# Optimization experiments

Measured on AMD Instinct MI355X. Metric: run time of the kernel, lower is better.

## Reference

```python
import jax, jax.numpy as jnp
import numpy as np

B, S, D = 2, 2048, 2048
H, HKV, DH = 16, 4, 128   # query heads, kv heads, head dim
N_REP = H // HKV
ROPE_BASE = 10000.0


def rotate_half(x):
    x1, x2 = x[..., : DH // 2], x[..., DH // 2 :]
    return jnp.concatenate((-x2, x1), axis=-1)


def rope_tables(seq_len, dtype=jnp.float32):
    inv_freq = 1.0 / (ROPE_BASE ** (jnp.arange(0, DH, 2, dtype=jnp.float32) / DH))
    t = jnp.arange(seq_len, dtype=jnp.float32)
    freqs = jnp.outer(t, inv_freq)                 # [S, DH/2]
    emb = jnp.concatenate((freqs, freqs), axis=-1)  # [S, DH]
    return jnp.cos(emb).astype(dtype), jnp.sin(emb).astype(dtype)


def setup_inputs() -> dict:
    key = jax.random.key(0)
    k1, k2, k3, k4, k5 = jax.random.split(key, 5)
    scale = 1.0 / np.sqrt(D)
    return {
        "hidden_states": jax.random.normal(k1, (B, S, D), dtype=jnp.float32),
        "position_ids": jnp.tile(jnp.arange(S, dtype=jnp.int32)[None, :], (B, 1)),
        "wq": jax.random.normal(k2, (D, H * DH), dtype=jnp.float32) * scale,
        "wk": jax.random.normal(k3, (D, HKV * DH), dtype=jnp.float32) * scale,
        "wv": jax.random.normal(k4, (D, HKV * DH), dtype=jnp.float32) * scale,
        "wo": jax.random.normal(k5, (H * DH, D), dtype=jnp.float32) * scale,
    }


def reference(hidden_states, position_ids, wq, wk, wv, wo):
    x = hidden_states
    b, s, _ = x.shape

    # QKV projections -> [B, H(kv), S, DH]
    q = (x @ wq).reshape(b, s, H, DH).transpose(0, 2, 1, 3)
    k = (x @ wk).reshape(b, s, HKV, DH).transpose(0, 2, 1, 3)
    v = (x @ wv).reshape(b, s, HKV, DH).transpose(0, 2, 1, 3)

    # Rotary position embedding
    cos_t, sin_t = rope_tables(s, x.dtype)
    cos = cos_t[position_ids][:, None, :, :]  # [B,1,S,DH]
    sin = sin_t[position_ids][:, None, :, :]
    q = q * cos + rotate_half(q) * sin
    k = k * cos + rotate_half(k) * sin

    # GQA: repeat KV heads to match query heads
    k = jnp.repeat(k, N_REP, axis=1)  # [B,H,S,DH]
    v = jnp.repeat(v, N_REP, axis=1)

    # Causal SDPA
    scores = jnp.einsum("bhqd,bhkd->bhqk", q, k) / jnp.sqrt(
        jnp.asarray(DH, x.dtype)
    )
    causal = jnp.tril(jnp.ones((s, s), dtype=bool))
    scores = jnp.where(causal[None, None], scores, jnp.asarray(-1e9, x.dtype))
    attn = jax.nn.softmax(scores, axis=-1)
    out = jnp.einsum("bhqk,bhkd->bhqd", attn, v)  # [B,H,S,DH]

    out = out.transpose(0, 2, 1, 3).reshape(b, s, H * DH)
    return out @ wo
```

## Files before the change

### kernel.cpp

```cpp
#include <hip/hip_runtime.h>
#include <cmath>

typedef unsigned short u16;
typedef float floatx4 __attribute__((ext_vector_type(4)));
typedef short short8 __attribute__((ext_vector_type(8)));
typedef short short4v __attribute__((ext_vector_type(4)));
typedef __bf16 bf16x8 __attribute__((ext_vector_type(8)));

#define GLOBAL_AS __attribute__((address_space(1)))
#define LDS_AS __attribute__((address_space(3)))

#define S_LEN 2048
#define D_MODEL 2048
#define NH 16
#define NKV 4
#define DHEAD 128
#define SM_SCALE 0.08838834764831843f
#define K2 (SM_SCALE * 1.4426950408889634f)

__device__ __forceinline__ u16 f2bf(float f) {
    unsigned int u = __builtin_bit_cast(unsigned int, f);
    u += 0x7fffu + ((u >> 16) & 1u);
    return (u16)(u >> 16);
}
__device__ __forceinline__ u16 f2bfr(float f) {
    unsigned int u = __builtin_bit_cast(unsigned int, f);
    return (u16)((u + 0x8000u) >> 16);
}
__device__ __forceinline__ float bf2f(u16 x) {
    unsigned int u = ((unsigned int)x) << 16;
    return __builtin_bit_cast(float, u);
}
__device__ __forceinline__ floatx4 zf4() {
    floatx4 z; z[0] = 0.f; z[1] = 0.f; z[2] = 0.f; z[3] = 0.f; return z;
}
__device__ __forceinline__ floatx4 mfma16(short8 a, short8 b, floatx4 c) {
    return __builtin_amdgcn_mfma_f32_16x16x32_bf16(
        __builtin_bit_cast(bf16x8, a), __builtin_bit_cast(bf16x8, b), c, 0, 0, 0);
}
__device__ __forceinline__ floatx4 mfma16k16(short4v a, short4v b, floatx4 c) {
    return __builtin_amdgcn_mfma_f32_16x16x16bf16_1k(a, b, c, 0, 0, 0);
}
__device__ __forceinline__ void async16(const u16* g, u16* l) {
    __builtin_amdgcn_global_load_lds((GLOBAL_AS void*)g, (LDS_AS void*)l, 16, 0, 0);
}

__global__ void cast_tables_kernel(const float4* __restrict__ in, ushort4* __restrict__ out,
                                   float* __restrict__ cs_tab, float* __restrict__ sn_tab) {
    int bid = blockIdx.x;
    if (bid < 8192) {
        int i = bid * 256 + threadIdx.x;
        float4 v = in[i];
        ushort4 o;
        o.x = f2bf(v.x); o.y = f2bf(v.y); o.z = f2bf(v.z); o.w = f2bf(v.w);
        out[i] = o;
    } else {
        int idx = (bid - 8192) * 256 + threadIdx.x;
        int p = idx >> 6, jj = idx & 63;
        double e = (double)(2 * jj) / 128.0;
        double invf = pow(10000.0, -e);
        float arg = (float)p * (float)invf;
        cs_tab[idx] = (float)cos((double)arg);
        sn_tab[idx] = (float)sin((double)arg);
    }
}

__global__ void transpose_all_kernel(const float* __restrict__ wq, const float* __restrict__ wk,
                                     const float* __restrict__ wv, const float* __restrict__ wo,
                                     u16* __restrict__ Wqkv, u16* __restrict__ Wo) {
    __shared__ float tile[32][33];
    int x = blockIdx.x;
    const float* in; u16* out; int C, bx;
    if (x < 64)      { in = wq; out = Wqkv;                     C = 2048; bx = x * 32; }
    else if (x < 80) { in = wk; out = Wqkv + (size_t)2048*2048; C = 512;  bx = (x - 64) * 32; }
    else if (x < 96) { in = wv; out = Wqkv + (size_t)2560*2048; C = 512;  bx = (x - 80) * 32; }
    else             { in = wo; out = Wo;                       C = 2048; bx = (x - 96) * 32; }
    const int R = 2048;
    int tx = threadIdx.x & 31, ty = threadIdx.x >> 5;
    int by = blockIdx.y * 32;
#pragma unroll
    for (int i = 0; i < 32; i += 8)
        tile[ty + i][tx] = in[(size_t)(by + ty + i) * C + bx + tx];
    __syncthreads();
#pragma unroll
    for (int i = 0; i < 32; i += 8)
        out[(size_t)(bx + ty + i) * R + by + tx] = f2bf(tile[tx][ty + i]);
}

__global__ void rope_k_kernel(u16* __restrict__ Kb, const int* __restrict__ pos,
                              const float4* __restrict__ cs_tab,
                              const float4* __restrict__ sn_tab) {
    int idx = blockIdx.x * 256 + threadIdx.x;
    int j4 = idx & 15;
    int s = (idx >> 4) & 2047;
    int r = idx >> 15;
    int hh = r & 3, b = r >> 2;
    int p = pos[b * S_LEN + s];
    float4 cs = cs_tab[p * 16 + j4];
    float4 sn = sn_tab[p * 16 + j4];
    u16* base = Kb + (((size_t)(b * NKV + hh)) * S_LEN + s) * DHEAD + j4 * 4;
    ushort4 a = *(const ushort4*)(base);
    ushort4 c = *(const ushort4*)(base + 64);
    ushort4 oa, oc;
    float x1, x2;
    x1 = bf2f(a.x); x2 = bf2f(c.x); oa.x = f2bf(x1 * cs.x - x2 * sn.x); oc.x = f2bf(x2 * cs.x + x1 * sn.x);
    x1 = bf2f(a.y); x2 = bf2f(c.y); oa.y = f2bf(x1 * cs.y - x2 * sn.y); oc.y = f2bf(x2 * cs.y + x1 * sn.y);
    x1 = bf2f(a.z); x2 = bf2f(c.z); oa.z = f2bf(x1 * cs.z - x2 * sn.z); oc.z = f2bf(x2 * cs.z + x1 * sn.z);
    x1 = bf2f(a.w); x2 = bf2f(c.w); oa.w = f2bf(x1 * cs.w - x2 * sn.w); oc.w = f2bf(x2 * cs.w + x1 * sn.w);
    *(ushort4*)(base) = oa;
    *(ushort4*)(base + 64) = oc;
}

__device__ __forceinline__ void gemm_mainloop(const u16* __restrict__ A,
                                              const u16* __restrict__ Bt,
                                              int K, u16* ldsA, u16* ldsB,
                                              floatx4 acc[4][4]) {
    const int t = threadIdx.x;
    const int lane = t & 63, wave = t >> 6;
    const int wr = wave >> 1, wc = wave & 1;
    const int lr = lane & 15, q = lane >> 4;
    const int m0 = blockIdx.y * 128, n0 = blockIdx.x * 128;
    const int swz = lr & 7;

#pragma unroll
    for (int r = 0; r < 4; ++r)
#pragma unroll
        for (int c = 0; c < 4; ++c) acc[r][c] = zf4();

    for (int k0 = 0; k0 < K; k0 += 64) {
#pragma unroll
        for (int i = 0; i < 4; ++i) {
            int ci = i * 256 + t;
            int row = ci >> 3;
            int kc = ((ci & 7) ^ (row & 7)) << 3;
            async16(A + (size_t)(m0 + row) * K + k0 + kc, ldsA + (i * 256 + wave * 64) * 8);
            async16(Bt + (size_t)(n0 + row) * K + k0 + kc, ldsB + (i * 256 + wave * 64) * 8);
        }
        __syncthreads();
#pragma unroll
        for (int ks = 0; ks < 2; ++ks) {
            short8 af[4], bfr[4];
#pragma unroll
            for (int r = 0; r < 4; ++r)
                af[r] = *(const short8*)(ldsA + (wr * 64 + r * 16 + lr) * 64 +
                                         (((ks * 4 + q) ^ swz) << 3));
#pragma unroll
            for (int c = 0; c < 4; ++c)
                bfr[c] = *(const short8*)(ldsB + (wc * 64 + c * 16 + lr) * 64 +
                                          (((ks * 4 + q) ^ swz) << 3));
#pragma unroll
            for (int r = 0; r < 4; ++r)
#pragma unroll
                for (int c = 0; c < 4; ++c)
                    acc[r][c] = mfma16(af[r], bfr[c], acc[r][c]);
        }
        __syncthreads();
    }
}

__global__ void qkv_gemm_kernel(const u16* __restrict__ A, const u16* __restrict__ Bt,
                                u16* __restrict__ Qb, u16* __restrict__ Kb,
                                u16* __restrict__ Vt) {
    __shared__ u16 ldsA[128 * 64];
    __shared__ u16 ldsB[128 * 64];
    floatx4 acc[4][4];
    gemm_mainloop(A, Bt, D_MODEL, ldsA, ldsB, acc);

    const int t = threadIdx.x, lane = t & 63, wave = t >> 6;
    const int wr = wave >> 1, wc = wave & 1, lr = lane & 15, q = lane >> 4;
    const int m0 = blockIdx.y * 128 + wr * 64, n0 = blockIdx.x * 128 + wc * 64;
#pragma unroll
    for (int r = 0; r < 4; ++r)
#pragma unroll
        for (int c = 0; c < 4; ++c) {
            int gc = n0 + c * 16 + lr;
#pragma unroll
            for (int rr = 0; rr < 4; ++rr) {
                int grow = m0 + r * 16 + q * 4 + rr;
                int bb = grow >> 11, s = grow & 2047;
                u16 bv = f2bf(acc[r][c][rr]);
                int d = gc & 127;
                if (gc < 2048) {
                    int hh = gc >> 7;
                    Qb[(((size_t)(bb * NH + hh)) * S_LEN + s) * DHEAD + d] = bv;
                } else if (gc < 2560) {
                    int hh = (gc - 2048) >> 7;
                    Kb[(((size_t)(bb * NKV + hh)) * S_LEN + s) * DHEAD + d] = bv;
                } else {
                    int hh = (gc - 2560) >> 7;
                    int s2 = s ^ ((d & 8) >> 1);
                    Vt[(((size_t)(bb * NKV + hh)) * DHEAD + d) * S_LEN + s2] = bv;
                }
            }
        }
}

__global__ void out_gemm_kernel(const u16* __restrict__ A, const u16* __restrict__ Bt,
                                float* __restrict__ out) {
    __shared__ u16 ldsA[128 * 64];
    __shared__ u16 ldsB[128 * 64];
    floatx4 acc[4][4];
    gemm_mainloop(A, Bt, D_MODEL, ldsA, ldsB, acc);

    const int t = threadIdx.x, lane = t & 63, wave = t >> 6;
    const int wr = wave >> 1, wc = wave & 1, lr = lane & 15, q = lane >> 4;
    const int m0 = blockIdx.y * 128 + wr * 64, n0 = blockIdx.x * 128 + wc * 64;
#pragma unroll
    for (int r = 0; r < 4; ++r)
#pragma unroll
        for (int c = 0; c < 4; ++c) {
            int gc = n0 + c * 16 + lr;
#pragma unroll
            for (int rr = 0; rr < 4; ++rr) {
                int grow = m0 + r * 16 + q * 4 + rr;
                out[(size_t)grow * D_MODEL + gc] = acc[r][c][rr];
            }
        }
}

__global__ __launch_bounds__(256, 2) void fa_kernel(const u16* __restrict__ Qb,
                                                    const u16* __restrict__ Kb,
                                                    const u16* __restrict__ Vt,
                                                    u16* __restrict__ Ob,
                                                    const int* __restrict__ pos,
                                                    const float4* __restrict__ cs_tab,
                                                    const float4* __restrict__ sn_tab) {
    __shared__ u16 ldsK[2][64 * 128];
    __shared__ u16 ldsV[2][128 * 64];

    const int t = threadIdx.x, lane = t & 63, wave = t >> 6;
    const int lr = lane & 15, q = lane >> 4;
    const int swz = lr & 7;

    const int bid = blockIdx.x;
    const int bh = bid >> 4, p = bid & 15;
    const int qt0 = p, qt1 = 31 - p;
    const int b = bh >> 4, h = bh & 15;
    const int kvh = h >> 2;

    const u16* Kp = Kb + (size_t)(b * NKV + kvh) * S_LEN * DHEAD;
    const u16* Vp = Vt + (size_t)(b * NKV + kvh) * DHEAD * S_LEN;

    short8 qf0[4], qf1[4];
    auto load_rope_q = [&](int qt, short8 (&qf)[4]) {
        const u16* Qp = Qb + ((size_t)((b * NH + h) * S_LEN) + qt * 64 + wave * 16) * DHEAD;
#pragma unroll
        for (int kk = 0; kk < 4; ++kk)
            qf[kk] = *(const short8*)(Qp + (size_t)lr * DHEAD + kk * 32 + q * 8);
        const int srow = qt * 64 + wave * 16 + lr;
        const int pp = pos[b * S_LEN + srow];
#pragma unroll
        for (int kk = 0; kk < 2; ++kk)
#pragma unroll
            for (int h4 = 0; h4 < 2; ++h4) {
                float4 cs = cs_tab[pp * 16 + kk * 8 + q * 2 + h4];
                float4 sn = sn_tab[pp * 16 + kk * 8 + q * 2 + h4];
#pragma unroll
                for (int e = 0; e < 4; ++e) {
                    float cc = (&cs.x)[e], ss = (&sn.x)[e];
                    int ei = h4 * 4 + e;
                    float x1 = bf2f((u16)qf[kk][ei]);
                    float x2 = bf2f((u16)qf[kk + 2][ei]);
                    qf[kk][ei]     = (short)f2bf(x1 * cc - x2 * ss);
                    qf[kk + 2][ei] = (short)f2bf(x2 * cc + x1 * ss);
                }
            }
    };
    load_rope_q(qt0, qf0);
    load_rope_q(qt1, qf1);

    auto stage = [&](int kt, int bs) {
#pragma unroll
        for (int i = 0; i < 4; ++i) {
            int ci = i * 256 + t;
            int krow = ci >> 4, kc = ((ci & 15) ^ ((ci >> 4) & 7)) << 3;
            async16(Kp + (size_t)(kt * 64 + krow) * DHEAD + kc,
                    &ldsK[bs][(i * 256 + wave * 64) * 8]);
            int dh = ci >> 3, vc = ((ci & 7) ^ ((ci >> 3) & 7)) << 3;
            async16(Vp + (size_t)dh * S_LEN + kt * 64 + vc,
                    &ldsV[bs][(i * 256 + wave * 64) * 8]);
        }
    };

    floatx4 accO[8];
    float m_i, l_i;

    auto do_tile = [&](int kt, int qt_c, const short8 (&qfc)[4], int bs) {
        floatx4 sc[4];
        __builtin_amdgcn_s_setprio(1);
#pragma unroll
        for (int c = 0; c < 4; ++c) {
            sc[c] = zf4();
#pragma unroll
            for (int kk = 0; kk < 4; ++kk) {
                short8 kfr = *(const short8*)(&ldsK[bs][(c * 16 + lr) * DHEAD +
                                              (((kk * 4 + q) ^ swz) << 3)]);
                sc[c] = mfma16(kfr, qfc[kk], sc[c]);
            }
        }
        __builtin_amdgcn_s_setprio(0);

        if (kt == qt_c) {
            const int qrow = wave * 16 + lr;
#pragma unroll
            for (int c = 0; c < 4; ++c)
#pragma unroll
                for (int rr = 0; rr < 4; ++rr)
                    if (c * 16 + q * 4 + rr > qrow) sc[c][rr] = -3e38f;
        }

        float mx = -3e38f;
#pragma unroll
        for (int c = 0; c < 4; ++c)
#pragma unroll
            for (int rr = 0; rr < 4; ++rr) mx = fmaxf(mx, sc[c][rr]);
        mx = fmaxf(mx, __shfl_xor(mx, 16));
        mx = fmaxf(mx, __shfl_xor(mx, 32));
        float mnew = fmaxf(m_i, mx);
        float mk = mnew * K2;
        bool anyup = __any(mnew > m_i);
        float rs = 0.f;
#pragma unroll
        for (int c = 0; c < 4; ++c)
#pragma unroll
            for (int rr = 0; rr < 4; ++rr) {
                float pe = __builtin_amdgcn_exp2f(fmaf(sc[c][rr], K2, -mk));
                sc[c][rr] = pe;
                rs += pe;
            }
        rs += __shfl_xor(rs, 16);
        rs += __shfl_xor(rs, 32);
        if (anyup) {
            float alpha = __builtin_amdgcn_exp2f(fmaf(m_i, K2, -mk));
            l_i = l_i * alpha + rs;
#pragma unroll
            for (int d = 0; d < 8; ++d) accO[d] *= alpha;
        } else {
            l_i += rs;
        }
        m_i = mnew;

        short4v pb[4];
#pragma unroll
        for (int c = 0; c < 4; ++c) {
            pb[c][0] = (short)f2bfr(sc[c][0]);
            pb[c][1] = (short)f2bfr(sc[c][1]);
            pb[c][2] = (short)f2bfr(sc[c][2]);
            pb[c][3] = (short)f2bfr(sc[c][3]);
        }

        __builtin_amdgcn_s_setprio(1);
#pragma unroll
        for (int ks = 0; ks < 4; ++ks)
#pragma unroll
            for (int d = 0; d < 8; ++d) {
                short4v vf = *(const short4v*)(&ldsV[bs][(d * 16 + lr) * 64 +
                                               (((ks * 2 + (q >> 1)) ^ swz) << 3) +
                                               (((q ^ (lr >> 3)) & 1) << 2)]);
                accO[d] = mfma16k16(vf, pb[ks], accO[d]);
            }
        __builtin_amdgcn_s_setprio(0);
    };

    auto epilogue = [&](int qt_c) {
        const int tok = qt_c * 64 + wave * 16 + lr;
        const float inv = 1.0f / l_i;
        u16* orow = Ob + ((size_t)(b * S_LEN + tok)) * (NH * DHEAD) + h * DHEAD + q * 4;
#pragma unroll
        for (int d = 0; d < 8; ++d) {
            ushort4 o;
            o.x = f2bf(accO[d][0] * inv);
            o.y = f2bf(accO[d][1] * inv);
            o.z = f2bf(accO[d][2] * inv);
            o.w = f2bf(accO[d][3] * inv);
            *(ushort4*)(orow + d * 16) = o;
        }
    };

#pragma unroll
    for (int d = 0; d < 8; ++d) accO[d] = zf4();
    m_i = -3e38f; l_i = 0.f;

    int cur = 0;
    stage(0, 0);
    __syncthreads();

    for (int kt = 0; kt <= qt0; ++kt) {
        int nxt = cur ^ 1;
        int nk = (kt < qt0) ? kt + 1 : 0;
        stage(nk, nxt);
        do_tile(kt, qt0, qf0, cur);
        __syncthreads();
        cur = nxt;
    }
    epilogue(qt0);
#pragma unroll
    for (int d = 0; d < 8; ++d) accO[d] = zf4();
    m_i = -3e38f; l_i = 0.f;

    for (int kt = 0; kt <= qt1; ++kt) {
        int nxt = cur ^ 1;
        if (kt < qt1) stage(kt + 1, nxt);
        do_tile(kt, qt1, qf1, cur);
        __syncthreads();
        cur = nxt;
    }
    epilogue(qt1);
}

extern "C" void kernel_launch(void* const* d_in, const int* in_sizes, int n_in,
                              void* d_out, int out_size, void* d_ws, size_t ws_size,
                              hipStream_t stream) {
    const float* X  = (const float*)d_in[0];
    const int* pos  = (const int*)d_in[1];
    const float* wq = (const float*)d_in[2];
    const float* wk = (const float*)d_in[3];
    const float* wv = (const float*)d_in[4];
    const float* wo = (const float*)d_in[5];
    float* out = (float*)d_out;

    char* w = (char*)d_ws;
    u16* Xbf    = (u16*)(w);
    u16* Wqkv   = (u16*)(w + 16777216);
    u16* Wo     = (u16*)(w + 29360128);
    u16* Qb     = (u16*)(w + 37748736);
    u16* Kb     = (u16*)(w + 54525952);
    u16* Vt     = (u16*)(w + 58720256);
    u16* Ob     = (u16*)(w + 62914560);
    float* cst  = (float*)(w + 79691776);
    float* snt  = (float*)(w + 80216064);

    cast_tables_kernel<<<8704, 256, 0, stream>>>((const float4*)X, (ushort4*)Xbf, cst, snt);
    transpose_all_kernel<<<dim3(160, 64), 256, 0, stream>>>(wq, wk, wv, wo, Wqkv, Wo);
    qkv_gemm_kernel<<<dim3(24, 32), 256, 0, stream>>>(Xbf, Wqkv, Qb, Kb, Vt);
    rope_k_kernel<<<1024, 256, 0, stream>>>(Kb, pos, (const float4*)cst, (const float4*)snt);
    fa_kernel<<<512, 256, 0, stream>>>(Qb, Kb, Vt, Ob, pos, (const float4*)cst, (const float4*)snt);
    out_gemm_kernel<<<dim3(16, 32), 256, 0, stream>>>(Ob, Wo, out);
}
```

Baseline: 304.1 us.

## Process both query tiles in one shared KV loop to reuse staged K/V

Merges the two sequential per-query-tile KV loops into a single loop over KV tiles. Each staged K/V tile is now shared by both query tiles while the lower tile is still active, which roughly halves the K/V global loads and LDS staging for the overlapping range. The sync is also changed from __syncthreads to explicit vmcnt waits plus raw barriers, so the next tile's prefetch can stay in flight. In exchange it doubles the accumulator and score registers, which may lower occupancy, and the hand-written waitcnt counts must exactly match the outstanding async loads to stay correct.

```diff
diff --git a/kernel.cpp b/kernel.cpp
--- a/kernel.cpp
+++ b/kernel.cpp
@@ -282,33 +282,22 @@
         }
     };
 
-    floatx4 accO[8];
-    float m_i, l_i;
-
-    auto do_tile = [&](int kt, int qt_c, const short8 (&qfc)[4], int bs) {
-        floatx4 sc[4];
-        __builtin_amdgcn_s_setprio(1);
-#pragma unroll
-        for (int c = 0; c < 4; ++c) {
-            sc[c] = zf4();
-#pragma unroll
-            for (int kk = 0; kk < 4; ++kk) {
-                short8 kfr = *(const short8*)(&ldsK[bs][(c * 16 + lr) * DHEAD +
-                                              (((kk * 4 + q) ^ swz) << 3)]);
-                sc[c] = mfma16(kfr, qfc[kk], sc[c]);
-            }
-        }
-        __builtin_amdgcn_s_setprio(0);
-
-        if (kt == qt_c) {
-            const int qrow = wave * 16 + lr;
-#pragma unroll
-            for (int c = 0; c < 4; ++c)
-#pragma unroll
-                for (int rr = 0; rr < 4; ++rr)
-                    if (c * 16 + q * 4 + rr > qrow) sc[c][rr] = -3e38f;
-        }
-
+    floatx4 accO0[8], accO1[8];
+#pragma unroll
+    for (int d = 0; d < 8; ++d) { accO0[d] = zf4(); accO1[d] = zf4(); }
+    float m0v = -3e38f, l0v = 0.f, m1v = -3e38f, l1v = 0.f;
+
+    auto do_mask = [&](floatx4 (&sc)[4]) {
+        const int qrow = wave * 16 + lr;
+#pragma unroll
+        for (int c = 0; c < 4; ++c)
+#pragma unroll
+            for (int rr = 0; rr < 4; ++rr)
+                if (c * 16 + q * 4 + rr > qrow) sc[c][rr] = -3e38f;
+    };
+
+    auto softmax_pack = [&](floatx4 (&sc)[4], float& m_i, float& l_i,
+                            floatx4 (&accO)[8], short4v (&pb)[4]) {
         float mx = -3e38f;
 #pragma unroll
         for (int c = 0; c < 4; ++c)
@@ -339,8 +328,6 @@
             l_i += rs;
         }
         m_i = mnew;
-
-        short4v pb[4];
 #pragma unroll
         for (int c = 0; c < 4; ++c) {
             pb[c][0] = (short)f2bfr(sc[c][0]);
@@ -348,21 +335,84 @@
             pb[c][2] = (short)f2bfr(sc[c][2]);
             pb[c][3] = (short)f2bfr(sc[c][3]);
         }
+    };
+
+    asm volatile("s_waitcnt vmcnt(0)" ::: "memory");
+    stage(0, 0);
+    int cur = 0;
+
+    for (int kt = 0; kt <= qt1; ++kt) {
+        stage(kt < qt1 ? kt + 1 : 0, cur ^ 1);
+        asm volatile("s_waitcnt vmcnt(8)" ::: "memory");
+        __builtin_amdgcn_s_barrier();
+
+        const bool act0 = (kt <= qt0);
+        floatx4 sc0[4], sc1[4];
 
         __builtin_amdgcn_s_setprio(1);
-#pragma unroll
-        for (int ks = 0; ks < 4; ++ks)
-#pragma unroll
-            for (int d = 0; d < 8; ++d) {
-                short4v vf = *(const short4v*)(&ldsV[bs][(d * 16 + lr) * 64 +
-                                               (((ks * 2 + (q >> 1)) ^ swz) << 3) +
-                                               (((q ^ (lr >> 3)) & 1) << 2)]);
-                accO[d] = mfma16k16(vf, pb[ks], accO[d]);
-            }
+        if (act0) {
+#pragma unroll
+            for (int c = 0; c < 4; ++c) {
+                sc0[c] = zf4(); sc1[c] = zf4();
+#pragma unroll
+                for (int kk = 0; kk < 4; ++kk) {
+                    short8 kfr = *(const short8*)(&ldsK[cur][(c * 16 + lr) * DHEAD +
+                                                  (((kk * 4 + q) ^ swz) << 3)]);
+                    sc1[c] = mfma16(kfr, qf1[kk], sc1[c]);
+                    sc0[c] = mfma16(kfr, qf0[kk], sc0[c]);
+                }
+            }
+        } else {
+#pragma unroll
+            for (int c = 0; c < 4; ++c) {
+                sc1[c] = zf4();
+#pragma unroll
+                for (int kk = 0; kk < 4; ++kk) {
+                    short8 kfr = *(const short8*)(&ldsK[cur][(c * 16 + lr) * DHEAD +
+                                                  (((kk * 4 + q) ^ swz) << 3)]);
+                    sc1[c] = mfma16(kfr, qf1[kk], sc1[c]);
+                }
+            }
+        }
         __builtin_amdgcn_s_setprio(0);
-    };
-
-    auto epilogue = [&](int qt_c) {
+
+        if (kt == qt0) do_mask(sc0);
+        if (kt == qt1) do_mask(sc1);
+
+        short4v pb0[4], pb1[4];
+        softmax_pack(sc1, m1v, l1v, accO1, pb1);
+        if (act0) softmax_pack(sc0, m0v, l0v, accO0, pb0);
+
+        __builtin_amdgcn_s_setprio(1);
+        if (act0) {
+#pragma unroll
+            for (int ks = 0; ks < 4; ++ks)
+#pragma unroll
+                for (int d = 0; d < 8; ++d) {
+                    short4v vf = *(const short4v*)(&ldsV[cur][(d * 16 + lr) * 64 +
+                                                   (((ks * 2 + (q >> 1)) ^ swz) << 3) +
+                                                   (((q ^ (lr >> 3)) & 1) << 2)]);
+                    accO1[d] = mfma16k16(vf, pb1[ks], accO1[d]);
+                    accO0[d] = mfma16k16(vf, pb0[ks], accO0[d]);
+                }
+        } else {
+#pragma unroll
+            for (int ks = 0; ks < 4; ++ks)
+#pragma unroll
+                for (int d = 0; d < 8; ++d) {
+                    short4v vf = *(const short4v*)(&ldsV[cur][(d * 16 + lr) * 64 +
+                                                   (((ks * 2 + (q >> 1)) ^ swz) << 3) +
+                                                   (((q ^ (lr >> 3)) & 1) << 2)]);
+                    accO1[d] = mfma16k16(vf, pb1[ks], accO1[d]);
+                }
+        }
+        __builtin_amdgcn_s_setprio(0);
+
+        __builtin_amdgcn_s_barrier();
+        cur ^= 1;
+    }
+
+    auto epilogue = [&](int qt_c, floatx4 (&accO)[8], float l_i) {
         const int tok = qt_c * 64 + wave * 16 + lr;
         const float inv = 1.0f / l_i;
         u16* orow = Ob + ((size_t)(b * S_LEN + tok)) * (NH * DHEAD) + h * DHEAD + q * 4;
@@ -376,36 +426,9 @@
             *(ushort4*)(orow + d * 16) = o;
         }
     };
-
-#pragma unroll
-    for (int d = 0; d < 8; ++d) accO[d] = zf4();
-    m_i = -3e38f; l_i = 0.f;
-
-    int cur = 0;
-    stage(0, 0);
-    __syncthreads();
-
-    for (int kt = 0; kt <= qt0; ++kt) {
-        int nxt = cur ^ 1;
-        int nk = (kt < qt0) ? kt + 1 : 0;
-        stage(nk, nxt);
-        do_tile(kt, qt0, qf0, cur);
-        __syncthreads();
-        cur = nxt;
-    }
-    epilogue(qt0);
-#pragma unroll
-    for (int d = 0; d < 8; ++d) accO[d] = zf4();
-    m_i = -3e38f; l_i = 0.f;
-
-    for (int kt = 0; kt <= qt1; ++kt) {
-        int nxt = cur ^ 1;
-        if (kt < qt1) stage(kt + 1, nxt);
-        do_tile(kt, qt1, qf1, cur);
-        __syncthreads();
-        cur = nxt;
-    }
-    epilogue(qt1);
+    epilogue(qt0, accO0, l0v);
+    epilogue(qt1, accO1, l1v);
+    asm volatile("s_waitcnt vmcnt(0)" ::: "memory");
 }
 
 extern "C" void kernel_launch(void* const* d_in, const int* in_sizes, int n_in,
```

New measurement: 323.7 us. 6.4% more time.

## Use 128-row query tiles with 8 waves sharing K/V staging in flash attention

Applied to the files above, without the earlier changes.

The attention kernel moves from 4-wave blocks that each handled two 64-row query tiles (paired for causal balance) to 8-wave blocks that each handle one 128-row query tile. Each staged K/V tile is now shared by twice as many query rows, which halves the global-to-LDS traffic per query. Load balance now comes from reversing the tile order for half the heads rather than from pairing tiles inside a block. The causal mask is generalised to the last two key tiles. Block work is now uneven, and the larger blocks with a launch bound of 4 may restrict registers and occupancy.

```diff
diff --git a/kernel.cpp b/kernel.cpp
--- a/kernel.cpp
+++ b/kernel.cpp
@@ -218,7 +218,7 @@
         }
 }
 
-__global__ __launch_bounds__(256, 2) void fa_kernel(const u16* __restrict__ Qb,
+__global__ __launch_bounds__(512, 4) void fa_kernel(const u16* __restrict__ Qb,
                                                     const u16* __restrict__ Kb,
                                                     const u16* __restrict__ Vt,
                                                     u16* __restrict__ Ob,
@@ -233,21 +233,22 @@
     const int swz = lr & 7;
 
     const int bid = blockIdx.x;
-    const int bh = bid >> 4, p = bid & 15;
-    const int qt0 = p, qt1 = 31 - p;
+    const int bh = bid >> 4, jslot = bid & 15;
+    const int qt2 = (bh & 16) ? (15 - jslot) : jslot;
     const int b = bh >> 4, h = bh & 15;
     const int kvh = h >> 2;
 
     const u16* Kp = Kb + (size_t)(b * NKV + kvh) * S_LEN * DHEAD;
     const u16* Vp = Vt + (size_t)(b * NKV + kvh) * DHEAD * S_LEN;
-
-    short8 qf0[4], qf1[4];
-    auto load_rope_q = [&](int qt, short8 (&qf)[4]) {
-        const u16* Qp = Qb + ((size_t)((b * NH + h) * S_LEN) + qt * 64 + wave * 16) * DHEAD;
-#pragma unroll
-        for (int kk = 0; kk < 4; ++kk)
-            qf[kk] = *(const short8*)(Qp + (size_t)lr * DHEAD + kk * 32 + q * 8);
-        const int srow = qt * 64 + wave * 16 + lr;
+    const u16* Qp = Qb + ((size_t)((b * NH + h) * S_LEN) + qt2 * 128 + wave * 16) * DHEAD;
+
+    short8 qf[4];
+#pragma unroll
+    for (int kk = 0; kk < 4; ++kk)
+        qf[kk] = *(const short8*)(Qp + (size_t)lr * DHEAD + kk * 32 + q * 8);
+
+    {
+        const int srow = qt2 * 128 + wave * 16 + lr;
         const int pp = pos[b * S_LEN + srow];
 #pragma unroll
         for (int kk = 0; kk < 2; ++kk)
@@ -265,27 +266,34 @@
                     qf[kk + 2][ei] = (short)f2bf(x2 * cc + x1 * ss);
                 }
             }
+    }
+
+    auto stage = [&](int kt, int bs) {
+#pragma unroll
+        for (int i = 0; i < 2; ++i) {
+            int ci = i * 512 + t;
+            int krow = ci >> 4, kc = ((ci & 15) ^ (krow & 7)) << 3;
+            async16(Kp + (size_t)(kt * 64 + krow) * DHEAD + kc,
+                    &ldsK[bs][(i * 512 + wave * 64) * 8]);
+            int dh = ci >> 3, vc = ((ci & 7) ^ (dh & 7)) << 3;
+            async16(Vp + (size_t)dh * S_LEN + kt * 64 + vc,
+                    &ldsV[bs][(i * 512 + wave * 64) * 8]);
+        }
     };
-    load_rope_q(qt0, qf0);
-    load_rope_q(qt1, qf1);
-
-    auto stage = [&](int kt, int bs) {
-#pragma unroll
-        for (int i = 0; i < 4; ++i) {
-            int ci = i * 256 + t;
-            int krow = ci >> 4, kc = ((ci & 15) ^ ((ci >> 4) & 7)) << 3;
-            async16(Kp + (size_t)(kt * 64 + krow) * DHEAD + kc,
-                    &ldsK[bs][(i * 256 + wave * 64) * 8]);
-            int dh = ci >> 3, vc = ((ci & 7) ^ ((ci >> 3) & 7)) << 3;
-            async16(Vp + (size_t)dh * S_LEN + kt * 64 + vc,
-                    &ldsV[bs][(i * 256 + wave * 64) * 8]);
-        }
-    };
 
     floatx4 accO[8];
-    float m_i, l_i;
-
-    auto do_tile = [&](int kt, int qt_c, const short8 (&qfc)[4], int bs) {
+#pragma unroll
+    for (int d = 0; d < 8; ++d) accO[d] = zf4();
+    float m_i = -3e38f, l_i = 0.f;
+
+    const int nkt = 2 * qt2 + 2;
+    int cur = 0;
+    stage(0, 0);
+    __syncthreads();
+
+    for (int kt = 0; kt < nkt; ++kt) {
+        if (kt + 1 < nkt) stage(kt + 1, cur ^ 1);
+
         floatx4 sc[4];
         __builtin_amdgcn_s_setprio(1);
 #pragma unroll
@@ -293,20 +301,21 @@
             sc[c] = zf4();
 #pragma unroll
             for (int kk = 0; kk < 4; ++kk) {
-                short8 kfr = *(const short8*)(&ldsK[bs][(c * 16 + lr) * DHEAD +
+                short8 kfr = *(const short8*)(&ldsK[cur][(c * 16 + lr) * DHEAD +
                                               (((kk * 4 + q) ^ swz) << 3)]);
-                sc[c] = mfma16(kfr, qfc[kk], sc[c]);
+                sc[c] = mfma16(kfr, qf[kk], sc[c]);
             }
         }
         __builtin_amdgcn_s_setprio(0);
 
-        if (kt == qt_c) {
-            const int qrow = wave * 16 + lr;
+        if (kt >= 2 * qt2) {
+            const int koff = (kt - 2 * qt2) << 6;
+            const int gq = wave * 16 + lr;
 #pragma unroll
             for (int c = 0; c < 4; ++c)
 #pragma unroll
                 for (int rr = 0; rr < 4; ++rr)
-                    if (c * 16 + q * 4 + rr > qrow) sc[c][rr] = -3e38f;
+                    if (koff + c * 16 + q * 4 + rr > gq) sc[c][rr] = -3e38f;
         }
 
         float mx = -3e38f;
@@ -354,58 +363,29 @@
         for (int ks = 0; ks < 4; ++ks)
 #pragma unroll
             for (int d = 0; d < 8; ++d) {
-                short4v vf = *(const short4v*)(&ldsV[bs][(d * 16 + lr) * 64 +
+                short4v vf = *(const short4v*)(&ldsV[cur][(d * 16 + lr) * 64 +
                                                (((ks * 2 + (q >> 1)) ^ swz) << 3) +
                                                (((q ^ (lr >> 3)) & 1) << 2)]);
                 accO[d] = mfma16k16(vf, pb[ks], accO[d]);
             }
         __builtin_amdgcn_s_setprio(0);
-    };
-
-    auto epilogue = [&](int qt_c) {
-        const int tok = qt_c * 64 + wave * 16 + lr;
-        const float inv = 1.0f / l_i;
-        u16* orow = Ob + ((size_t)(b * S_LEN + tok)) * (NH * DHEAD) + h * DHEAD + q * 4;
-#pragma unroll
-        for (int d = 0; d < 8; ++d) {
-            ushort4 o;
-            o.x = f2bf(accO[d][0] * inv);
-            o.y = f2bf(accO[d][1] * inv);
-            o.z = f2bf(accO[d][2] * inv);
-            o.w = f2bf(accO[d][3] * inv);
-            *(ushort4*)(orow + d * 16) = o;
-        }
-    };
-
-#pragma unroll
-    for (int d = 0; d < 8; ++d) accO[d] = zf4();
-    m_i = -3e38f; l_i = 0.f;
-
-    int cur = 0;
-    stage(0, 0);
-    __syncthreads();
-
-    for (int kt = 0; kt <= qt0; ++kt) {
-        int nxt = cur ^ 1;
-        int nk = (kt < qt0) ? kt + 1 : 0;
-        stage(nk, nxt);
-        do_tile(kt, qt0, qf0, cur);
+
         __syncthreads();
-        cur = nxt;
+        cur ^= 1;
     }
-    epilogue(qt0);
-#pragma unroll
-    for (int d = 0; d < 8; ++d) accO[d] = zf4();
-    m_i = -3e38f; l_i = 0.f;
-
-    for (int kt = 0; kt <= qt1; ++kt) {
-        int nxt = cur ^ 1;
-        if (kt < qt1) stage(kt + 1, nxt);
-        do_tile(kt, qt1, qf1, cur);
-        __syncthreads();
-        cur = nxt;
+
+    const int tok = qt2 * 128 + wave * 16 + lr;
+    const float inv = 1.0f / l_i;
+    u16* orow = Ob + ((size_t)(b * S_LEN + tok)) * (NH * DHEAD) + h * DHEAD + q * 4;
+#pragma unroll
+    for (int d = 0; d < 8; ++d) {
+        ushort4 o;
+        o.x = f2bf(accO[d][0] * inv);
+        o.y = f2bf(accO[d][1] * inv);
+        o.z = f2bf(accO[d][2] * inv);
+        o.w = f2bf(accO[d][3] * inv);
+        *(ushort4*)(orow + d * 16) = o;
     }
-    epilogue(qt1);
 }
 
 extern "C" void kernel_launch(void* const* d_in, const int* in_sizes, int n_in,
@@ -434,6 +414,6 @@
     transpose_all_kernel<<<dim3(160, 64), 256, 0, stream>>>(wq, wk, wv, wo, Wqkv, Wo);
     qkv_gemm_kernel<<<dim3(24, 32), 256, 0, stream>>>(Xbf, Wqkv, Qb, Kb, Vt);
     rope_k_kernel<<<1024, 256, 0, stream>>>(Kb, pos, (const float4*)cst, (const float4*)snt);
-    fa_kernel<<<512, 256, 0, stream>>>(Qb, Kb, Vt, Ob, pos, (const float4*)cst, (const float4*)snt);
+    fa_kernel<<<512, 512, 0, stream>>>(Qb, Kb, Vt, Ob, pos, (const float4*)cst, (const float4*)snt);
     out_gemm_kernel<<<dim3(16, 32), 256, 0, stream>>>(Ob, Wo, out);
 }
```

New measurement: 297.9 us. 1.02x faster.

## Double-buffer GEMM mainloop with larger 8-wave tiles and MFMA priority

Applied to the files above, without the earlier changes.

Replaces the single-buffered 128x128 GEMM mainloop with a templated 8-wave version that prefetches the next K tile into a second LDS buffer while computing the current one, synchronised with explicit vmcnt waits and raw barriers. Tiles grow to 256x256 for the QKV projection and 128x256 for the output projection. MFMA blocks are wrapped in s_setprio. The aim is to hide global-load latency and raise operand reuse per block. In exchange there are fewer blocks, which can underfill the CUs (192 and 256 blocks), plus higher register pressure and hand-tuned vmcnt counts that must match the issued loads exactly.

```diff
diff --git a/kernel.cpp b/kernel.cpp
--- a/kernel.cpp
+++ b/kernel.cpp
@@ -111,66 +111,111 @@
     *(ushort4*)(base + 64) = oc;
 }
 
-__device__ __forceinline__ void gemm_mainloop(const u16* __restrict__ A,
-                                              const u16* __restrict__ Bt,
-                                              int K, u16* ldsA, u16* ldsB,
-                                              floatx4 acc[4][4]) {
+template <int M_REP>
+__device__ __forceinline__ void gemm_mainloop8(const u16* __restrict__ A,
+                                               const u16* __restrict__ Bt,
+                                               int K,
+                                               u16* ldsA0, u16* ldsB0,
+                                               u16* ldsA1, u16* ldsB1,
+                                               floatx4 acc[M_REP][4]) {
     const int t = threadIdx.x;
     const int lane = t & 63, wave = t >> 6;
-    const int wr = wave >> 1, wc = wave & 1;
+    const int wr = wave >> 2, wc = wave & 3;
     const int lr = lane & 15, q = lane >> 4;
-    const int m0 = blockIdx.y * 128, n0 = blockIdx.x * 128;
     const int swz = lr & 7;
-
-#pragma unroll
-    for (int r = 0; r < 4; ++r)
+    const int m0 = blockIdx.y * (M_REP * 32), n0 = blockIdx.x * 256;
+
+#pragma unroll
+    for (int r = 0; r < M_REP; ++r)
 #pragma unroll
         for (int c = 0; c < 4; ++c) acc[r][c] = zf4();
 
-    for (int k0 = 0; k0 < K; k0 += 64) {
-#pragma unroll
-        for (int i = 0; i < 4; ++i) {
-            int ci = i * 256 + t;
+    auto stage = [&](int kt, u16* la, u16* lb) {
+        const int k0 = kt * 64;
+#pragma unroll
+        for (int i = 0; i < M_REP / 2; ++i) {
+            int ci = i * 512 + t;
             int row = ci >> 3;
             int kc = ((ci & 7) ^ (row & 7)) << 3;
-            async16(A + (size_t)(m0 + row) * K + k0 + kc, ldsA + (i * 256 + wave * 64) * 8);
-            async16(Bt + (size_t)(n0 + row) * K + k0 + kc, ldsB + (i * 256 + wave * 64) * 8);
-        }
-        __syncthreads();
-#pragma unroll
-        for (int ks = 0; ks < 2; ++ks) {
-            short8 af[4], bfr[4];
-#pragma unroll
-            for (int r = 0; r < 4; ++r)
-                af[r] = *(const short8*)(ldsA + (wr * 64 + r * 16 + lr) * 64 +
-                                         (((ks * 4 + q) ^ swz) << 3));
-#pragma unroll
-            for (int c = 0; c < 4; ++c)
-                bfr[c] = *(const short8*)(ldsB + (wc * 64 + c * 16 + lr) * 64 +
-                                          (((ks * 4 + q) ^ swz) << 3));
-#pragma unroll
-            for (int r = 0; r < 4; ++r)
+            async16(A + (size_t)(m0 + row) * K + k0 + kc, la + (i * 512 + wave * 64) * 8);
+        }
+#pragma unroll
+        for (int i = 0; i < 4; ++i) {
+            int ci = i * 512 + t;
+            int row = ci >> 3;
+            int kc = ((ci & 7) ^ (row & 7)) << 3;
+            async16(Bt + (size_t)(n0 + row) * K + k0 + kc, lb + (i * 512 + wave * 64) * 8);
+        }
+    };
+
+    auto compute = [&](const u16* la, const u16* lb) {
+        short8 bfr[4][2];
+#pragma unroll
+        for (int c = 0; c < 4; ++c)
+#pragma unroll
+            for (int ks = 0; ks < 2; ++ks)
+                bfr[c][ks] = *(const short8*)(lb + (wc * 64 + c * 16 + lr) * 64 +
+                                              (((ks * 4 + q) ^ swz) << 3));
+#pragma unroll
+        for (int p = 0; p < M_REP / 2; ++p) {
+            short8 af[2][2];
+#pragma unroll
+            for (int rr2 = 0; rr2 < 2; ++rr2)
+#pragma unroll
+                for (int ks = 0; ks < 2; ++ks)
+                    af[rr2][ks] = *(const short8*)(la + (wr * (M_REP * 16) +
+                                                   (2 * p + rr2) * 16 + lr) * 64 +
+                                                   (((ks * 4 + q) ^ swz) << 3));
+            __builtin_amdgcn_s_setprio(1);
+#pragma unroll
+            for (int rr2 = 0; rr2 < 2; ++rr2)
 #pragma unroll
                 for (int c = 0; c < 4; ++c)
-                    acc[r][c] = mfma16(af[r], bfr[c], acc[r][c]);
-        }
-        __syncthreads();
+#pragma unroll
+                    for (int ks = 0; ks < 2; ++ks)
+                        acc[2 * p + rr2][c] =
+                            mfma16(af[rr2][ks], bfr[c][ks], acc[2 * p + rr2][c]);
+            __builtin_amdgcn_s_setprio(0);
+        }
+    };
+
+    auto waitN = [&]() {
+        if constexpr (M_REP == 8) asm volatile("s_waitcnt vmcnt(8)" ::: "memory");
+        else                      asm volatile("s_waitcnt vmcnt(6)" ::: "memory");
+    };
+
+    const int NT = K / 64;
+    stage(0, ldsA0, ldsB0);
+    for (int kt = 0; kt < NT; kt += 2) {
+        stage(kt + 1, ldsA1, ldsB1);
+        waitN();
+        __builtin_amdgcn_s_barrier();
+        compute(ldsA0, ldsB0);
+        __builtin_amdgcn_s_barrier();
+        stage(kt + 2 < NT ? kt + 2 : 0, ldsA0, ldsB0);
+        waitN();
+        __builtin_amdgcn_s_barrier();
+        compute(ldsA1, ldsB1);
+        __builtin_amdgcn_s_barrier();
     }
-}
-
-__global__ void qkv_gemm_kernel(const u16* __restrict__ A, const u16* __restrict__ Bt,
-                                u16* __restrict__ Qb, u16* __restrict__ Kb,
-                                u16* __restrict__ Vt) {
-    __shared__ u16 ldsA[128 * 64];
-    __shared__ u16 ldsB[128 * 64];
-    floatx4 acc[4][4];
-    gemm_mainloop(A, Bt, D_MODEL, ldsA, ldsB, acc);
+    asm volatile("s_waitcnt vmcnt(0)" ::: "memory");
+}
+
+__global__ __launch_bounds__(512, 1) void qkv_gemm_kernel(const u16* __restrict__ A,
+                                                          const u16* __restrict__ Bt,
+                                                          u16* __restrict__ Qb,
+                                                          u16* __restrict__ Kb,
+                                                          u16* __restrict__ Vt) {
+    __shared__ u16 ldsA[2][256 * 64];
+    __shared__ u16 ldsB[2][256 * 64];
+    floatx4 acc[8][4];
+    gemm_mainloop8<8>(A, Bt, D_MODEL, ldsA[0], ldsB[0], ldsA[1], ldsB[1], acc);
 
     const int t = threadIdx.x, lane = t & 63, wave = t >> 6;
-    const int wr = wave >> 1, wc = wave & 1, lr = lane & 15, q = lane >> 4;
-    const int m0 = blockIdx.y * 128 + wr * 64, n0 = blockIdx.x * 128 + wc * 64;
-#pragma unroll
-    for (int r = 0; r < 4; ++r)
+    const int wr = wave >> 2, wc = wave & 3, lr = lane & 15, q = lane >> 4;
+    const int m0 = blockIdx.y * 256 + wr * 128, n0 = blockIdx.x * 256 + wc * 64;
+#pragma unroll
+    for (int r = 0; r < 8; ++r)
 #pragma unroll
         for (int c = 0; c < 4; ++c) {
             int gc = n0 + c * 16 + lr;
@@ -195,16 +240,17 @@
         }
 }
 
-__global__ void out_gemm_kernel(const u16* __restrict__ A, const u16* __restrict__ Bt,
-                                float* __restrict__ out) {
-    __shared__ u16 ldsA[128 * 64];
-    __shared__ u16 ldsB[128 * 64];
+__global__ __launch_bounds__(512, 1) void out_gemm_kernel(const u16* __restrict__ A,
+                                                          const u16* __restrict__ Bt,
+                                                          float* __restrict__ out) {
+    __shared__ u16 ldsA[2][128 * 64];
+    __shared__ u16 ldsB[2][256 * 64];
     floatx4 acc[4][4];
-    gemm_mainloop(A, Bt, D_MODEL, ldsA, ldsB, acc);
+    gemm_mainloop8<4>(A, Bt, D_MODEL, ldsA[0], ldsB[0], ldsA[1], ldsB[1], acc);
 
     const int t = threadIdx.x, lane = t & 63, wave = t >> 6;
-    const int wr = wave >> 1, wc = wave & 1, lr = lane & 15, q = lane >> 4;
-    const int m0 = blockIdx.y * 128 + wr * 64, n0 = blockIdx.x * 128 + wc * 64;
+    const int wr = wave >> 2, wc = wave & 3, lr = lane & 15, q = lane >> 4;
+    const int m0 = blockIdx.y * 128 + wr * 64, n0 = blockIdx.x * 256 + wc * 64;
 #pragma unroll
     for (int r = 0; r < 4; ++r)
 #pragma unroll
@@ -432,8 +478,8 @@
 
     cast_tables_kernel<<<8704, 256, 0, stream>>>((const float4*)X, (ushort4*)Xbf, cst, snt);
     transpose_all_kernel<<<dim3(160, 64), 256, 0, stream>>>(wq, wk, wv, wo, Wqkv, Wo);
-    qkv_gemm_kernel<<<dim3(24, 32), 256, 0, stream>>>(Xbf, Wqkv, Qb, Kb, Vt);
+    qkv_gemm_kernel<<<dim3(12, 16), 512, 0, stream>>>(Xbf, Wqkv, Qb, Kb, Vt);
     rope_k_kernel<<<1024, 256, 0, stream>>>(Kb, pos, (const float4*)cst, (const float4*)snt);
     fa_kernel<<<512, 256, 0, stream>>>(Qb, Kb, Vt, Ob, pos, (const float4*)cst, (const float4*)snt);
-    out_gemm_kernel<<<dim3(16, 32), 256, 0, stream>>>(Ob, Wo, out);
-}
+    out_gemm_kernel<<<dim3(8, 32), 512, 0, stream>>>(Ob, Wo, out);
+}
```

New measurement: 316.1 us. +3.9%, slower.
